# Optimization experiments

Measured on AMD Instinct MI355X. Metric: run time of the kernel, lower is better.

Reference implementation:

```python
import jax, jax.numpy as jnp
import numpy as np

EPS = 1e-12

def _l2n(x):
    return x / jnp.sqrt(jnp.maximum(jnp.sum(x * x, axis=-1, keepdims=True), EPS))

def _sn_kernel(w, u):
    # One power iteration of spectral normalization (TF SpectralNormalization._compute_weights).
    wr = w.reshape(-1, w.shape[-1])           # [in, out] (1x1 conv kernel flattened)
    v = _l2n(u @ wr.T)                        # [1, in]
    u2 = _l2n(v @ wr)                         # [1, out]
    u2 = jax.lax.stop_gradient(u2)
    v = jax.lax.stop_gradient(v)
    sigma = (v @ wr) @ u2.T                   # [1, 1]
    return w / sigma[0, 0]

def setup_inputs() -> dict:
    key = jax.random.key(0)
    ks = jax.random.split(key, 14)
    B, H, W, C = 8, 64, 64, 256
    d = C // 8
    inp = {
        'x':  jax.random.normal(ks[0], (B, H, W, C), jnp.float32),
        'wf': jax.random.normal(ks[1], (C, d), jnp.float32) * 0.02,
        'bf': jax.random.normal(ks[2], (d,), jnp.float32) * 0.02,
        'uf': jax.random.normal(ks[3], (1, d), jnp.float32) * 0.02,
        'wg': jax.random.normal(ks[4], (C, d), jnp.float32) * 0.02,
        'bg': jax.random.normal(ks[5], (d,), jnp.float32) * 0.02,
        'ug': jax.random.normal(ks[6], (1, d), jnp.float32) * 0.02,
        'wh': jax.random.normal(ks[7], (C, d), jnp.float32) * 0.02,
        'bh': jax.random.normal(ks[8], (d,), jnp.float32) * 0.02,
        'uh': jax.random.normal(ks[9], (1, d), jnp.float32) * 0.02,
        'wv': jax.random.normal(ks[10], (d, C), jnp.float32) * 0.02,
        'bv': jax.random.normal(ks[11], (C,), jnp.float32) * 0.02,
        'uv': jax.random.normal(ks[12], (1, C), jnp.float32) * 0.02,
        'gamma': jax.random.normal(ks[13], (1,), jnp.float32) * 0.1,
    }
    return inp

def reference(x, wf, bf, uf, wg, bg, ug, wh, bh, uh, wv, bv, uv, gamma):
    B, H, W, C = x.shape
    N = H * W
    # spectrally-normalized 1x1 conv kernels
    kf = _sn_kernel(wf, uf)
    kg = _sn_kernel(wg, ug)
    kh = _sn_kernel(wh, uh)
    kv = _sn_kernel(wv, uv)
    # 1x1 convs == channel matmuls on flattened spatial dims
    xf = x.reshape(B, N, C)
    f = xf @ kf + bf            # [B, N, d]
    g = xf @ kg + bg            # [B, N, d]
    h = xf @ kh + bh            # [B, N, d]
    s = jnp.einsum('bnd,bmd->bnm', g, f)   # [B, N, N]
    beta = jax.nn.softmax(s, axis=-1)
    v = jnp.einsum('bnm,bmd->bnd', beta, h)  # [B, N, d]
    o = v @ kv + bv             # [B, N, C]
    out = gamma[0] * o.reshape(B, H, W, C) + x
    return out
```

## Files before the change

kernel.cpp:

```cpp
#include <hip/hip_runtime.h>
#include <math.h>

typedef __attribute__((ext_vector_type(8))) short bf16x8;
typedef __attribute__((ext_vector_type(4))) short bf16x4;
typedef __attribute__((ext_vector_type(4))) float f32x4;

#define LOG2E 1.4426950408889634f

#if __has_builtin(__builtin_amdgcn_exp2f)
#define EXP2(x) __builtin_amdgcn_exp2f(x)
#else
#define EXP2(x) exp2f(x)
#endif

static __device__ __forceinline__ short f2bf(float f) {
  unsigned u = __builtin_bit_cast(unsigned, f);
  u = u + 0x7FFFu + ((u >> 16) & 1u);
  return (short)(u >> 16);
}

__global__ __launch_bounds__(256) void proj_fused(
    const float* __restrict__ x,
    const float* __restrict__ wf, const float* __restrict__ bf_,
    const float* __restrict__ uf,
    const float* __restrict__ wg, const float* __restrict__ bg_,
    const float* __restrict__ ug,
    const float* __restrict__ wh, const float* __restrict__ bh_,
    const float* __restrict__ uh,
    short* __restrict__ fo, short* __restrict__ go, short* __restrict__ hto) {
  __shared__ __align__(16) short wt[96 * 256];
  __shared__ float scl[3];
  int tid = threadIdx.x;
  int wave = tid >> 6, lane = tid & 63;
  int quad = lane >> 4, l16 = lane & 15;
  int row0 = blockIdx.x * 64;

  const float* xr = x + (size_t)(row0 + wave * 16 + l16) * 256 + quad * 8;
  bf16x8 afv[8];
#pragma unroll
  for (int k8 = 0; k8 < 8; k8++) {
    float4 a0 = *(const float4*)(xr + k8 * 32);
    float4 a1 = *(const float4*)(xr + k8 * 32 + 4);
    bf16x8 a;
    a[0] = f2bf(a0.x); a[1] = f2bf(a0.y); a[2] = f2bf(a0.z); a[3] = f2bf(a0.w);
    a[4] = f2bf(a1.x); a[5] = f2bf(a1.y); a[6] = f2bf(a1.z); a[7] = f2bf(a1.w);
    afv[k8] = a;
  }

  float* red = (float*)wt;
  float* sv = (float*)wt + 256;
#pragma unroll 1
  for (int sel = 0; sel < 3; sel++) {
    const float* w = (sel == 0) ? wf : (sel == 1) ? wg : wh;
    const float* u = (sel == 0) ? uf : (sel == 1) ? ug : uh;
    float t = 0.f;
#pragma unroll
    for (int j = 0; j < 32; j++) t += u[j] * w[tid * 32 + j];
    float v2 = t * t;
#pragma unroll
    for (int off = 32; off > 0; off >>= 1) v2 += __shfl_xor(v2, off);
    if (lane == 0) red[wave] = v2;
    __syncthreads();
    float nv = sqrtf(fmaxf(red[0] + red[1] + red[2] + red[3], 1e-12f));
    sv[tid] = t / nv;
    __syncthreads();
    int c = tid & 31, part = tid >> 5;
    float p = 0.f;
#pragma unroll
    for (int k = 0; k < 32; k++) {
      int i = part * 32 + k;
      p += sv[i] * w[i * 32 + c];
    }
    red[tid] = p;
    __syncthreads();
    float q2 = 0.f;
    if (tid < 32) {
      float s_c = 0.f;
#pragma unroll
      for (int pp = 0; pp < 8; pp++) s_c += red[tid + 32 * pp];
      q2 = s_c * s_c;
    }
#pragma unroll
    for (int off = 32; off > 0; off >>= 1) q2 += __shfl_xor(q2, off);
    if (tid == 0) {
      float s2 = q2;
      float sig = s2 / sqrtf(fmaxf(s2, 1e-12f));
      float s = 1.0f / sig;
      if (sel == 1) s *= LOG2E;
      scl[sel] = s;
    }
    __syncthreads();
  }

  float s0 = scl[0], s1 = scl[1], s2v = scl[2];
#pragma unroll 1
  for (int c0 = 0; c0 < 96; c0++) {
    int se = c0 >> 5, cc = c0 & 31;
    const float* w = (se == 0) ? wf : (se == 1) ? wg : wh;
    float sc_ = (se == 0) ? s0 : (se == 1) ? s1 : s2v;
    wt[c0 * 256 + (tid ^ ((c0 & 15) << 3))] = f2bf(w[tid * 32 + cc] * sc_);
  }
  __syncthreads();

  f32x4 acc[6];
#pragma unroll
  for (int t = 0; t < 6; t++) acc[t] = (f32x4){0.f, 0.f, 0.f, 0.f};
#pragma unroll
  for (int k8 = 0; k8 < 8; k8++) {
    int kc = k8 * 32;
#pragma unroll
    for (int t = 0; t < 6; t++) {
      int rw = t * 16 + l16;
      bf16x8 bfr =
          *(const bf16x8*)&wt[rw * 256 + ((kc + quad * 8) ^ (l16 << 3))];
      acc[t] =
          __builtin_amdgcn_mfma_f32_16x16x32_bf16(afv[k8], bfr, acc[t], 0, 0, 0);
    }
  }
  __syncthreads();

  float* hsh = (float*)wt;
  int b = row0 >> 12;
  int n0 = row0 & 4095;
  int rbase = row0 + wave * 16;
#pragma unroll
  for (int t = 0; t < 4; t++) {
    int c = t * 16 + l16;
    int se = c >> 5, cc = c & 31;
    float bb = se ? (bg_[cc] * LOG2E) : bf_[cc];
    short* dst = se ? go : fo;
#pragma unroll
    for (int r = 0; r < 4; r++) {
      int row = rbase + quad * 4 + r;
      dst[(size_t)row * 32 + cc] = f2bf(acc[t][r] + bb);
    }
  }
#pragma unroll
  for (int t = 4; t < 6; t++) {
    int cc = (t - 4) * 16 + l16;
    float bb = bh_[cc];
#pragma unroll
    for (int r = 0; r < 4; r++)
      hsh[(wave * 16 + quad * 4 + r) * 33 + cc] = acc[t][r] + bb;
  }
  __syncthreads();
  {
    int d = tid >> 3, ng = tid & 7;
    bf16x8 tmp;
#pragma unroll
    for (int i = 0; i < 8; i++) tmp[i] = f2bf(hsh[(ng * 8 + i) * 33 + d]);
    *(bf16x8*)(hto + (size_t)(b * 32 + d) * 4096 + n0 + ng * 8) = tmp;
  }
}

__global__ __launch_bounds__(256, 4) void attn_kernel(
    const short* __restrict__ g_, const short* __restrict__ f_,
    const short* __restrict__ ht_, short* __restrict__ po,
    float* __restrict__ ls) {
  __shared__ __align__(16) short psh[4][4][16][72];
  int b = blockIdx.y;
  int z = blockIdx.z;
  int wave = threadIdx.x >> 6;
  int lane = threadIdx.x & 63;
  int quad = lane >> 4, l16 = lane & 15;
  int qbase = blockIdx.x * 256 + wave * 64;
  int kc0 = z * 512;

  const short* fb = f_ + (size_t)b * 4096 * 32;
  const short* hb = ht_ + (size_t)b * 32 * 4096;

  bf16x8 ga[4];
#pragma unroll
  for (int grp = 0; grp < 4; grp++)
    ga[grp] = *(const bf16x8*)(g_ + (size_t)(b * 4096 + qbase + grp * 16 + l16) * 32 +
                               quad * 8);

  f32x4 oacc[4][2];
  f32x4 lacc[4];
#pragma unroll
  for (int grp = 0; grp < 4; grp++) {
#pragma unroll
    for (int dt = 0; dt < 2; dt++) oacc[grp][dt] = (f32x4){0.f, 0.f, 0.f, 0.f};
    lacc[grp] = (f32x4){0.f, 0.f, 0.f, 0.f};
  }

  short onev = (l16 == 0) ? (short)0x3F80 : (short)0;
  bf16x8 aones = {onev, onev, onev, onev, onev, onev, onev, onev};

  for (int kc = kc0; kc < kc0 + 512; kc += 64) {
    bf16x8 F[4];
#pragma unroll
    for (int t = 0; t < 4; t++)
      F[t] = *(const bf16x8*)(fb + (size_t)(kc + t * 16 + l16) * 32 + quad * 8);
    bf16x8 H[2][2];
#pragma unroll
    for (int half = 0; half < 2; half++)
#pragma unroll
      for (int dt = 0; dt < 2; dt++)
        H[half][dt] = *(const bf16x8*)(hb + (size_t)(dt * 16 + l16) * 4096 +
                                       kc + half * 32 + quad * 8);

#pragma unroll
    for (int g = 0; g < 4; g++) {
      f32x4 s[4];
#pragma unroll
      for (int t = 0; t < 4; t++)
        s[t] = __builtin_amdgcn_mfma_f32_16x16x32_bf16(
            F[t], ga[g], (f32x4){0.f, 0.f, 0.f, 0.f}, 0, 0, 0);

      unsigned long long* prow64 = (unsigned long long*)&psh[wave][g][l16][0];
#pragma unroll
      for (int t = 0; t < 4; t++) {
        float p0 = EXP2(s[t][0]);
        float p1 = EXP2(s[t][1]);
        float p2 = EXP2(s[t][2]);
        float p3 = EXP2(s[t][3]);
        unsigned lo = __builtin_amdgcn_perm(__builtin_bit_cast(unsigned, p1),
                                            __builtin_bit_cast(unsigned, p0),
                                            0x07060302u);
        unsigned hi = __builtin_amdgcn_perm(__builtin_bit_cast(unsigned, p3),
                                            __builtin_bit_cast(unsigned, p2),
                                            0x07060302u);
        prow64[4 * t + quad] = ((unsigned long long)hi << 32) | lo;
      }
      asm volatile("" ::: "memory");

#pragma unroll
      for (int half = 0; half < 2; half++) {
        bf16x8 pa = *(const bf16x8*)(&psh[wave][g][l16][half * 32 + quad * 8]);
#pragma unroll
        for (int dt = 0; dt < 2; dt++)
          oacc[g][dt] = __builtin_amdgcn_mfma_f32_16x16x32_bf16(
              H[half][dt], pa, oacc[g][dt], 0, 0, 0);
        lacc[g] = __builtin_amdgcn_mfma_f32_16x16x32_bf16(aones, pa, lacc[g],
                                                          0, 0, 0);
      }
      asm volatile("" ::: "memory");
    }
  }

#pragma unroll
  for (int grp = 0; grp < 4; grp++) {
    size_t row = (size_t)b * 4096 + qbase + grp * 16 + l16;
    short* pod = po + ((size_t)z * 32768 + row) * 32;
#pragma unroll
    for (int dt = 0; dt < 2; dt++) {
      unsigned w0 = (unsigned)(unsigned short)f2bf(oacc[grp][dt][0]) |
                    ((unsigned)(unsigned short)f2bf(oacc[grp][dt][1]) << 16);
      unsigned w1 = (unsigned)(unsigned short)f2bf(oacc[grp][dt][2]) |
                    ((unsigned)(unsigned short)f2bf(oacc[grp][dt][3]) << 16);
      unsigned* dst = (unsigned*)(pod + dt * 16 + quad * 4);
      dst[0] = w0;
      dst[1] = w1;
    }
  }
  if (quad == 0) {
#pragma unroll
    for (int grp = 0; grp < 4; grp++)
      ls[(size_t)z * 32768 + (size_t)b * 4096 + qbase + grp * 16 + l16] =
          lacc[grp][0];
  }
}

__global__ __launch_bounds__(256) void outproj_fused(
    const short* __restrict__ po, const float* __restrict__ ls,
    const float* __restrict__ wv, const float* __restrict__ uv,
    const float* __restrict__ bv, const float* __restrict__ gamma,
    const float* __restrict__ x, float* __restrict__ out) {
  __shared__ __align__(16) float osh[4][16][260];
  short* kv = (short*)osh;
  float* redp = (float*)((char*)osh + 20480);
  float* svv = (float*)((char*)osh + 21504);
  float* sclv = (float*)((char*)osh + 21632);
  int tid = threadIdx.x;
  int wave = tid >> 6, lane = tid & 63;
  int quad = lane >> 4, l16 = lane & 15;

  {
    int i = tid >> 3, p8 = tid & 7;
    float pv = 0.f;
#pragma unroll
    for (int k = 0; k < 32; k++) {
      int j = p8 * 32 + k;
      pv += uv[j] * wv[i * 256 + j];
    }
    redp[tid] = pv;
    __syncthreads();
    float vi = 0.f;
    if (tid < 32) {
#pragma unroll
      for (int p = 0; p < 8; p++) vi += redp[tid * 8 + p];
    }
    float q2 = (tid < 32) ? vi * vi : 0.f;
#pragma unroll
    for (int off = 32; off > 0; off >>= 1) q2 += __shfl_xor(q2, off);
    if (tid == 0) sclv[0] = sqrtf(fmaxf(q2, 1e-12f));
    __syncthreads();
    if (tid < 32) svv[tid] = vi / sclv[0];
    __syncthreads();
    float yc = 0.f;
#pragma unroll
    for (int i2 = 0; i2 < 32; i2++) yc += svv[i2] * wv[i2 * 256 + tid];
    float q3 = yc * yc;
#pragma unroll
    for (int off = 32; off > 0; off >>= 1) q3 += __shfl_xor(q3, off);
    if (lane == 0) redp[wave] = q3;
    __syncthreads();
    if (tid == 0) {
      float s2 = redp[0] + redp[1] + redp[2] + redp[3];
      float sig = s2 / sqrtf(fmaxf(s2, 1e-12f));
      sclv[1] = 1.0f / sig;
    }
    __syncthreads();
    float scv = sclv[1];
#pragma unroll
    for (int i2 = 0; i2 < 32; i2++)
      kv[tid * 40 + i2] = f2bf(wv[i2 * 256 + tid] * scv);
  }
  __syncthreads();

  int row0 = blockIdx.x * 64;
  int rbase = row0 + wave * 16;
  size_t row = (size_t)rbase + l16;

  float vacc[8];
#pragma unroll
  for (int j = 0; j < 8; j++) vacc[j] = 0.f;
  float l = 0.f;
#pragma unroll
  for (int z = 0; z < 8; z++) {
    const unsigned* p =
        (const unsigned*)(po + ((size_t)z * 32768 + row) * 32 + quad * 8);
#pragma unroll
    for (int j = 0; j < 4; j++) {
      unsigned w = p[j];
      vacc[2 * j] += __builtin_bit_cast(float, w << 16);
      vacc[2 * j + 1] += __builtin_bit_cast(float, w & 0xFFFF0000u);
    }
    l += ls[(size_t)z * 32768 + row];
  }
  float inv = 1.0f / l;
  bf16x8 va;
#pragma unroll
  for (int j = 0; j < 8; j++) va[j] = f2bf(vacc[j] * inv);

  float gm = gamma[0];

  f32x4 acc[16];
#pragma unroll
  for (int t = 0; t < 16; t++) {
    bf16x8 kf = *(const bf16x8*)&kv[(t * 16 + l16) * 40 + quad * 8];
    acc[t] = __builtin_amdgcn_mfma_f32_16x16x32_bf16(
        va, kf, (f32x4){0.f, 0.f, 0.f, 0.f}, 0, 0, 0);
  }
  __syncthreads();

#pragma unroll
  for (int t = 0; t < 16; t++) {
    float bb = bv[t * 16 + l16];
#pragma unroll
    for (int r = 0; r < 4; r++) {
      osh[wave][quad * 4 + r][t * 16 + l16] = acc[t][r] + bb;
    }
  }
  asm volatile("" ::: "memory");
  {
    int r_l = lane >> 2, c_l = lane & 3;
    int orow = row0 + wave * 16 + r_l;
    const float* oshr = &osh[wave][r_l][0];
    const float4* xr = (const float4*)(x + (size_t)orow * 256);
    float4* outr = (float4*)(out + (size_t)orow * 256);
#pragma unroll
    for (int i = 0; i < 16; i++) {
      int c4 = c_l + i * 4;
      float4 o4 = *(const float4*)&oshr[c4 * 4];
      float4 xv = xr[c4];
      float4 ov;
      ov.x = gm * o4.x + xv.x;
      ov.y = gm * o4.y + xv.y;
      ov.z = gm * o4.z + xv.z;
      ov.w = gm * o4.w + xv.w;
      outr[c4] = ov;
    }
  }
}

extern "C" void kernel_launch(void* const* d_in, const int* in_sizes, int n_in,
                              void* d_out, int out_size, void* d_ws,
                              size_t ws_size, hipStream_t stream) {
  const float* x = (const float*)d_in[0];
  const float* wf = (const float*)d_in[1];
  const float* bf = (const float*)d_in[2];
  const float* uf = (const float*)d_in[3];
  const float* wg = (const float*)d_in[4];
  const float* bg = (const float*)d_in[5];
  const float* ug = (const float*)d_in[6];
  const float* wh = (const float*)d_in[7];
  const float* bh = (const float*)d_in[8];
  const float* uh = (const float*)d_in[9];
  const float* wv = (const float*)d_in[10];
  const float* bv = (const float*)d_in[11];
  const float* uv = (const float*)d_in[12];
  const float* gamma = (const float*)d_in[13];
  float* out = (float*)d_out;

  char* ws = (char*)d_ws;
  short* fo = (short*)(ws + 2u * 1024 * 1024);
  short* go = (short*)(ws + 4u * 1024 * 1024);
  short* hto = (short*)(ws + 6u * 1024 * 1024);
  short* po = (short*)(ws + 10u * 1024 * 1024);
  float* lsp = (float*)(ws + 26u * 1024 * 1024);

  proj_fused<<<512, 256, 0, stream>>>(x, wf, bf, uf, wg, bg, ug, wh, bh, uh,
                                      fo, go, hto);
  attn_kernel<<<dim3(16, 8, 8), 256, 0, stream>>>(go, fo, hto, po, lsp);
  outproj_fused<<<512, 256, 0, stream>>>(po, lsp, wv, uv, bv, gamma, x, out);
}
```

Baseline: 189.9 us.

## Halve attention per-wave query tile, double grid, and cache weight rows in registers

The attention kernel now gives each wave 32 query rows instead of 64. It doubles the grid to 2048 blocks and raises the occupancy hint to 8 blocks per SM, with one shared P tile per wave. Separately, the projection kernel loads each thread's weight row into registers once with float4 loads and reuses it for the power iteration and for the scaled bf16 weight writes. It also moves the reduction scratch out of the weight tile. The change aims at better latency hiding and fewer global weight reads, but each F/H load now feeds half as much compute, roughly doubling K/V traffic.

```diff
diff --git a/kernel.cpp b/kernel.cpp
--- a/kernel.cpp
+++ b/kernel.cpp
@@ -29,6 +29,8 @@
     const float* __restrict__ uh,
     short* __restrict__ fo, short* __restrict__ go, short* __restrict__ hto) {
   __shared__ __align__(16) short wt[96 * 256];
+  __shared__ float red[256];
+  __shared__ float svx[256];
   __shared__ float scl[3];
   int tid = threadIdx.x;
   int wave = tid >> 6, lane = tid & 63;
@@ -47,29 +49,38 @@
     afv[k8] = a;
   }
 
-  float* red = (float*)wt;
-  float* sv = (float*)wt + 256;
 #pragma unroll 1
   for (int sel = 0; sel < 3; sel++) {
     const float* w = (sel == 0) ? wf : (sel == 1) ? wg : wh;
     const float* u = (sel == 0) ? uf : (sel == 1) ? ug : uh;
+
+    float wr[32];
+    {
+      const float4* wrow = (const float4*)(w + tid * 32);
+#pragma unroll
+      for (int q4 = 0; q4 < 8; q4++) {
+        float4 v = wrow[q4];
+        wr[4 * q4 + 0] = v.x; wr[4 * q4 + 1] = v.y;
+        wr[4 * q4 + 2] = v.z; wr[4 * q4 + 3] = v.w;
+      }
+    }
     float t = 0.f;
 #pragma unroll
-    for (int j = 0; j < 32; j++) t += u[j] * w[tid * 32 + j];
+    for (int j = 0; j < 32; j++) t += u[j] * wr[j];
     float v2 = t * t;
 #pragma unroll
     for (int off = 32; off > 0; off >>= 1) v2 += __shfl_xor(v2, off);
     if (lane == 0) red[wave] = v2;
     __syncthreads();
     float nv = sqrtf(fmaxf(red[0] + red[1] + red[2] + red[3], 1e-12f));
-    sv[tid] = t / nv;
+    svx[tid] = t / nv;
     __syncthreads();
     int c = tid & 31, part = tid >> 5;
     float p = 0.f;
 #pragma unroll
     for (int k = 0; k < 32; k++) {
       int i = part * 32 + k;
-      p += sv[i] * w[i * 32 + c];
+      p += svx[i] * w[i * 32 + c];
     }
     red[tid] = p;
     __syncthreads();
@@ -90,17 +101,13 @@
       scl[sel] = s;
     }
     __syncthreads();
-  }
-
-  float s0 = scl[0], s1 = scl[1], s2v = scl[2];
-#pragma unroll 1
-  for (int c0 = 0; c0 < 96; c0++) {
-    int se = c0 >> 5, cc = c0 & 31;
-    const float* w = (se == 0) ? wf : (se == 1) ? wg : wh;
-    float sc_ = (se == 0) ? s0 : (se == 1) ? s1 : s2v;
-    wt[c0 * 256 + (tid ^ ((c0 & 15) << 3))] = f2bf(w[tid * 32 + cc] * sc_);
-  }
-  __syncthreads();
+    float s = scl[sel];
+#pragma unroll
+    for (int cc = 0; cc < 32; cc++) {
+      wt[(sel * 32 + cc) * 256 + (tid ^ ((cc & 15) << 3))] = f2bf(wr[cc] * s);
+    }
+    __syncthreads();
+  }
 
   f32x4 acc[6];
 #pragma unroll
@@ -153,32 +160,32 @@
   }
 }
 
-__global__ __launch_bounds__(256, 4) void attn_kernel(
+__global__ __launch_bounds__(256, 8) void attn_kernel(
     const short* __restrict__ g_, const short* __restrict__ f_,
     const short* __restrict__ ht_, short* __restrict__ po,
     float* __restrict__ ls) {
-  __shared__ __align__(16) short psh[4][4][16][72];
+  __shared__ __align__(16) short psh[4][16][72];
   int b = blockIdx.y;
   int z = blockIdx.z;
   int wave = threadIdx.x >> 6;
   int lane = threadIdx.x & 63;
   int quad = lane >> 4, l16 = lane & 15;
-  int qbase = blockIdx.x * 256 + wave * 64;
+  int qbase = blockIdx.x * 128 + wave * 32;
   int kc0 = z * 512;
 
   const short* fb = f_ + (size_t)b * 4096 * 32;
   const short* hb = ht_ + (size_t)b * 32 * 4096;
 
-  bf16x8 ga[4];
-#pragma unroll
-  for (int grp = 0; grp < 4; grp++)
+  bf16x8 ga[2];
+#pragma unroll
+  for (int grp = 0; grp < 2; grp++)
     ga[grp] = *(const bf16x8*)(g_ + (size_t)(b * 4096 + qbase + grp * 16 + l16) * 32 +
                                quad * 8);
 
-  f32x4 oacc[4][2];
-  f32x4 lacc[4];
-#pragma unroll
-  for (int grp = 0; grp < 4; grp++) {
+  f32x4 oacc[2][2];
+  f32x4 lacc[2];
+#pragma unroll
+  for (int grp = 0; grp < 2; grp++) {
 #pragma unroll
     for (int dt = 0; dt < 2; dt++) oacc[grp][dt] = (f32x4){0.f, 0.f, 0.f, 0.f};
     lacc[grp] = (f32x4){0.f, 0.f, 0.f, 0.f};
@@ -201,14 +208,14 @@
                                        kc + half * 32 + quad * 8);
 
 #pragma unroll
-    for (int g = 0; g < 4; g++) {
+    for (int g = 0; g < 2; g++) {
       f32x4 s[4];
 #pragma unroll
       for (int t = 0; t < 4; t++)
         s[t] = __builtin_amdgcn_mfma_f32_16x16x32_bf16(
             F[t], ga[g], (f32x4){0.f, 0.f, 0.f, 0.f}, 0, 0, 0);
 
-      unsigned long long* prow64 = (unsigned long long*)&psh[wave][g][l16][0];
+      unsigned long long* prow64 = (unsigned long long*)&psh[wave][l16][0];
 #pragma unroll
       for (int t = 0; t < 4; t++) {
         float p0 = EXP2(s[t][0]);
@@ -227,7 +234,7 @@
 
 #pragma unroll
       for (int half = 0; half < 2; half++) {
-        bf16x8 pa = *(const bf16x8*)(&psh[wave][g][l16][half * 32 + quad * 8]);
+        bf16x8 pa = *(const bf16x8*)(&psh[wave][l16][half * 32 + quad * 8]);
 #pragma unroll
         for (int dt = 0; dt < 2; dt++)
           oacc[g][dt] = __builtin_amdgcn_mfma_f32_16x16x32_bf16(
@@ -240,7 +247,7 @@
   }
 
 #pragma unroll
-  for (int grp = 0; grp < 4; grp++) {
+  for (int grp = 0; grp < 2; grp++) {
     size_t row = (size_t)b * 4096 + qbase + grp * 16 + l16;
     short* pod = po + ((size_t)z * 32768 + row) * 32;
 #pragma unroll
@@ -256,7 +263,7 @@
   }
   if (quad == 0) {
 #pragma unroll
-    for (int grp = 0; grp < 4; grp++)
+    for (int grp = 0; grp < 2; grp++)
       ls[(size_t)z * 32768 + (size_t)b * 4096 + qbase + grp * 16 + l16] =
           lacc[grp][0];
   }
@@ -413,6 +420,6 @@
 
   proj_fused<<<512, 256, 0, stream>>>(x, wf, bf, uf, wg, bg, ug, wh, bh, uh,
                                       fo, go, hto);
-  attn_kernel<<<dim3(16, 8, 8), 256, 0, stream>>>(go, fo, hto, po, lsp);
+  attn_kernel<<<dim3(32, 8, 8), 256, 0, stream>>>(go, fo, hto, po, lsp);
   outproj_fused<<<512, 256, 0, stream>>>(po, lsp, wv, uv, bv, gamma, x, out);
 }
```

Measured after the change: 267.9 us. +41.1%, slower.
